# Performance work log

Hardware: AMD Instinct MI355X
Metric: run time of the kernel (lower is better)

The kernel has to match this reference:

```python
import jax, jax.numpy as jnp
import numpy as np

N = 33554432  # 2**25 elements

def setup_inputs() -> dict:
    key = jax.random.key(0)
    kx, ky = jax.random.split(key)
    x = jax.random.normal(kx, (N,), dtype=jnp.float32)
    y = jax.random.normal(ky, (N,), dtype=jnp.float32)
    return {"x": x, "y": y}

def reference(x, y):
    # abs_diff = |x - y|; rel_diff = abs_diff / y if y != 0 else abs_diff
    abs_diff = jnp.abs(x - y)
    safe_y = jnp.where(y == 0, 1.0, y)  # avoid div-by-zero NaNs in the masked branch
    rel_diff = jnp.where(y == 0, abs_diff, abs_diff / safe_y)
    # mean over N (module returns the mean; the variance it computes is discarded)
    return jnp.sum(rel_diff) / rel_diff.shape[0]
```

## Files before the change

### kernel.cpp

```cpp
#include <hip/hip_runtime.h>

#define TPB 256
#define NBLK 2048

__device__ __forceinline__ double rel_term(float x, float y) {
    float d = fabsf(x - y);
    float r = (y == 0.0f) ? d : d / y;
    return (double)r;
}

__global__ __launch_bounds__(TPB) void rdl_partial_kernel(
    const float4* __restrict__ x, const float4* __restrict__ y,
    double* __restrict__ partial, int nvec) {
    double acc = 0.0;
    int idx = blockIdx.x * TPB + threadIdx.x;
    int stride = gridDim.x * TPB;
    for (int i = idx; i < nvec; i += stride) {
        float4 xv = x[i];
        float4 yv = y[i];
        acc += rel_term(xv.x, yv.x);
        acc += rel_term(xv.y, yv.y);
        acc += rel_term(xv.z, yv.z);
        acc += rel_term(xv.w, yv.w);
    }
    for (int off = 32; off > 0; off >>= 1)
        acc += __shfl_down(acc, off, 64);
    __shared__ double smem[TPB / 64];
    int lane = threadIdx.x & 63;
    int wid  = threadIdx.x >> 6;
    if (lane == 0) smem[wid] = acc;
    __syncthreads();
    if (threadIdx.x == 0) {
        double s = 0.0;
        #pragma unroll
        for (int w = 0; w < TPB / 64; ++w) s += smem[w];
        partial[blockIdx.x] = s;
    }
}

__global__ __launch_bounds__(TPB) void rdl_final_kernel(
    const double* __restrict__ partial, float* __restrict__ out,
    int nblocks, double invN) {
    double acc = 0.0;
    for (int i = threadIdx.x; i < nblocks; i += TPB)
        acc += partial[i];
    for (int off = 32; off > 0; off >>= 1)
        acc += __shfl_down(acc, off, 64);
    __shared__ double smem[TPB / 64];
    int lane = threadIdx.x & 63;
    int wid  = threadIdx.x >> 6;
    if (lane == 0) smem[wid] = acc;
    __syncthreads();
    if (threadIdx.x == 0) {
        double s = 0.0;
        #pragma unroll
        for (int w = 0; w < TPB / 64; ++w) s += smem[w];
        out[0] = (float)(s * invN);
    }
}

extern "C" void kernel_launch(void* const* d_in, const int* in_sizes, int n_in,
                              void* d_out, int out_size, void* d_ws, size_t ws_size,
                              hipStream_t stream) {
    const float* x = (const float*)d_in[0];
    const float* y = (const float*)d_in[1];
    int n = in_sizes[0];
    int nvec = n / 4;
    double* partial = (double*)d_ws;

    rdl_partial_kernel<<<NBLK, TPB, 0, stream>>>(
        (const float4*)x, (const float4*)y, partial, nvec);
    rdl_final_kernel<<<1, TPB, 0, stream>>>(
        partial, (float*)d_out, NBLK, 1.0 / (double)n);
}
```

Baseline: 277.0 us.

## Unroll loads 8x with split accumulators, fast reciprocal, and larger grid

Restructures the grid-stride loop so each thread issues 8 float4 loads per array before computing, which raises memory-level parallelism. Four independent double accumulators break the FP64 add dependency chain. The IEEE divide is replaced with a hardware reciprocal approximation followed by a multiply, which trades a little precision for fewer instructions. The grid grows to up to 4096 blocks depending on workspace size.

```diff
diff --git a/kernel.cpp b/kernel.cpp
--- a/kernel.cpp
+++ b/kernel.cpp
@@ -1,28 +1,40 @@
 #include <hip/hip_runtime.h>
 
 #define TPB 256
-#define NBLK 2048
+#define NBLK_MAX 4096
 
-__device__ __forceinline__ double rel_term(float x, float y) {
+__device__ __forceinline__ float relf(float x, float y) {
     float d = fabsf(x - y);
-    float r = (y == 0.0f) ? d : d / y;
-    return (double)r;
+    float r = d * __builtin_amdgcn_rcpf(y);
+    return (y == 0.0f) ? d : r;
 }
 
-__global__ __launch_bounds__(TPB) void rdl_partial_kernel(
+__device__ __forceinline__ double term4(float4 xv, float4 yv) {
+    return ((double)relf(xv.x, yv.x) + (double)relf(xv.y, yv.y))
+         + ((double)relf(xv.z, yv.z) + (double)relf(xv.w, yv.w));
+}
+
+__global__ __launch_bounds__(TPB, 4) void rdl_partial_kernel(
     const float4* __restrict__ x, const float4* __restrict__ y,
     double* __restrict__ partial, int nvec) {
-    double acc = 0.0;
-    int idx = blockIdx.x * TPB + threadIdx.x;
+    double accd[4] = {0.0, 0.0, 0.0, 0.0};
+    int tid = blockIdx.x * TPB + threadIdx.x;
     int stride = gridDim.x * TPB;
-    for (int i = idx; i < nvec; i += stride) {
-        float4 xv = x[i];
-        float4 yv = y[i];
-        acc += rel_term(xv.x, yv.x);
-        acc += rel_term(xv.y, yv.y);
-        acc += rel_term(xv.z, yv.z);
-        acc += rel_term(xv.w, yv.w);
+
+    int i = tid;
+    for (; i + 7 * stride < nvec; i += 8 * stride) {
+        float4 xv[8], yv[8];
+        #pragma unroll
+        for (int u = 0; u < 8; ++u) xv[u] = x[i + u * stride];
+        #pragma unroll
+        for (int u = 0; u < 8; ++u) yv[u] = y[i + u * stride];
+        #pragma unroll
+        for (int u = 0; u < 8; ++u) accd[u & 3] += term4(xv[u], yv[u]);
     }
+    for (; i < nvec; i += stride) accd[0] += term4(x[i], y[i]);
+
+    double acc = (accd[0] + accd[1]) + (accd[2] + accd[3]);
+
     for (int off = 32; off > 0; off >>= 1)
         acc += __shfl_down(acc, off, 64);
     __shared__ double smem[TPB / 64];
@@ -66,10 +78,15 @@
     const float* y = (const float*)d_in[1];
     int n = in_sizes[0];
     int nvec = n / 4;
+
+    int nblk = (int)(ws_size / sizeof(double));
+    if (nblk > NBLK_MAX) nblk = NBLK_MAX;
+    if (nblk < 1) nblk = 1;
+
     double* partial = (double*)d_ws;
 
-    rdl_partial_kernel<<<NBLK, TPB, 0, stream>>>(
+    rdl_partial_kernel<<<nblk, TPB, 0, stream>>>(
         (const float4*)x, (const float4*)y, partial, nvec);
     rdl_final_kernel<<<1, TPB, 0, stream>>>(
-        partial, (float*)d_out, NBLK, 1.0 / (double)n);
+        partial, (float*)d_out, nblk, 1.0 / (double)n);
 }
```

After: 288.8 us. 1.04x slower.

## Stage loads through LDS via global_load_lds and use fast reciprocal with float partials

Applied to the files above, without the earlier changes.

Rewrites the partial-sum kernel to pull 4 float4 chunks per thread of x and y directly into LDS with the global_load_lds builtin, then reads them back and computes the terms. Per-element double accumulation becomes float partial sums folded into a double once per chunk, and true division is replaced by an approximate reciprocal multiply. Block count drops from 2048 to 1024. It aims to get more bytes in flight and cut ALU cost, but adds LDS round trips and barriers, and the approximate reciprocal changes accuracy slightly.

```diff
diff --git a/kernel.cpp b/kernel.cpp
--- a/kernel.cpp
+++ b/kernel.cpp
@@ -1,39 +1,75 @@
 #include <hip/hip_runtime.h>
 
 #define TPB 256
-#define NBLK 2048
+#define U 4
+#define CHUNK (TPB * U)
+#define NBLK 1024
 
-__device__ __forceinline__ double rel_term(float x, float y) {
+typedef __attribute__((address_space(1))) const void* gas_ptr;
+typedef __attribute__((address_space(3))) void* las_ptr;
+
+__device__ __forceinline__ float relf(float x, float y) {
     float d = fabsf(x - y);
-    float r = (y == 0.0f) ? d : d / y;
-    return (double)r;
+    float r = d * __builtin_amdgcn_rcpf(y);
+    return (y == 0.0f) ? d : r;
 }
 
 __global__ __launch_bounds__(TPB) void rdl_partial_kernel(
     const float4* __restrict__ x, const float4* __restrict__ y,
     double* __restrict__ partial, int nvec) {
-    double acc = 0.0;
-    int idx = blockIdx.x * TPB + threadIdx.x;
-    int stride = gridDim.x * TPB;
-    for (int i = idx; i < nvec; i += stride) {
-        float4 xv = x[i];
-        float4 yv = y[i];
-        acc += rel_term(xv.x, yv.x);
-        acc += rel_term(xv.y, yv.y);
-        acc += rel_term(xv.z, yv.z);
-        acc += rel_term(xv.w, yv.w);
+
+    __shared__ float4 lx[U][TPB];
+    __shared__ float4 ly[U][TPB];
+
+    const int t = threadIdx.x;
+    const int w = t >> 6;
+    double accd = 0.0;
+
+    const int nchunk = nvec / CHUNK;
+    for (int c = blockIdx.x; c < nchunk; c += gridDim.x) {
+        const int base = c * CHUNK;
+        __syncthreads();
+        #pragma unroll
+        for (int u = 0; u < U; ++u)
+            __builtin_amdgcn_global_load_lds(
+                (gas_ptr)(x + base + u * TPB + t),
+                (las_ptr)&lx[u][w * 64], 16, 0, 0);
+        #pragma unroll
+        for (int u = 0; u < U; ++u)
+            __builtin_amdgcn_global_load_lds(
+                (gas_ptr)(y + base + u * TPB + t),
+                (las_ptr)&ly[u][w * 64], 16, 0, 0);
+        __syncthreads();
+
+        float a0 = 0.f, a1 = 0.f;
+        #pragma unroll
+        for (int u = 0; u < U; ++u) {
+            float4 xv = lx[u][t];
+            float4 yv = ly[u][t];
+            a0 += relf(xv.x, yv.x) + relf(xv.z, yv.z);
+            a1 += relf(xv.y, yv.y) + relf(xv.w, yv.w);
+        }
+        accd += (double)(a0 + a1);
     }
+
+    for (int i = nchunk * CHUNK + blockIdx.x * TPB + t; i < nvec;
+         i += gridDim.x * TPB) {
+        float4 xv = x[i], yv = y[i];
+        accd += (double)(relf(xv.x, yv.x) + relf(xv.z, yv.z)
+                       + relf(xv.y, yv.y) + relf(xv.w, yv.w));
+    }
+
+    double acc = accd;
     for (int off = 32; off > 0; off >>= 1)
         acc += __shfl_down(acc, off, 64);
     __shared__ double smem[TPB / 64];
-    int lane = threadIdx.x & 63;
-    int wid  = threadIdx.x >> 6;
-    if (lane == 0) smem[wid] = acc;
+    int lane = t & 63;
+    if (lane == 0) smem[w] = acc;
     __syncthreads();
-    if (threadIdx.x == 0) {
+    if (t == 0) {
         double s = 0.0;
         #pragma unroll
-        for (int w = 0; w < TPB / 64; ++w) s += smem[w];
+        for (int wi = 0; wi < TPB / 64; ++wi) s += smem[wi];
         partial[blockIdx.x] = s;
     }
 }
@@ -66,6 +102,7 @@
     const float* y = (const float*)d_in[1];
     int n = in_sizes[0];
     int nvec = n / 4;
+
     double* partial = (double*)d_ws;
 
     rdl_partial_kernel<<<NBLK, TPB, 0, stream>>>(
```

New measurement: 274.6 us. Within noise of the previous version (-0.9%).
